# Kernel optimization log

Measured on AMD Instinct MI355X. Metric: run time of the kernel, lower is better.

Reference implementation:

```python
import jax, jax.numpy as jnp
import numpy as np

N_NODES = 100000
N_EDGES = 1600000
EMB_DIM = 128
BN_EPS = 1e-5


def setup_inputs() -> dict:
    key = jax.random.key(0)
    k = jax.random.split(key, 5)
    x = jax.random.normal(k[0], (N_NODES, EMB_DIM), dtype=jnp.float32)
    src = jax.random.randint(k[1], (N_EDGES,), 0, N_NODES)
    dst = jax.random.randint(k[2], (N_EDGES,), 0, N_NODES)
    W = jax.random.normal(k[3], (EMB_DIM, EMB_DIM), dtype=jnp.float32) / np.float32(np.sqrt(EMB_DIM))
    b = jnp.zeros((EMB_DIM,), dtype=jnp.float32)
    gamma = jnp.ones((EMB_DIM,), dtype=jnp.float32)
    beta = jnp.zeros((EMB_DIM,), dtype=jnp.float32)
    return {"x": x, "src": src, "dst": dst, "W": W, "b": b, "gamma": gamma, "beta": beta}


def reference(x, src, dst, W, b, gamma, beta):
    n = x.shape[0]
    ones = jnp.ones(src.shape, dtype=x.dtype)
    # DGL GraphConv norm='both': degrees clamped to min 1
    deg_out = jnp.maximum(jax.ops.segment_sum(ones, src, num_segments=n), 1.0)
    deg_in = jnp.maximum(jax.ops.segment_sum(ones, dst, num_segments=n), 1.0)
    norm_src = jax.lax.rsqrt(deg_out)  # [N]
    norm_dst = jax.lax.rsqrt(deg_in)   # [N]
    # W applied before aggregation (in_feats == out_feats path in DGL)
    h = (x * norm_src[:, None]) @ W                              # [N, D]
    agg = jax.ops.segment_sum(h[src], dst, num_segments=n)       # SpMM gather/scatter, [N, D]
    h = agg * norm_dst[:, None] + b                              # [N, D]
    # BatchNorm1d over nodes (training-mode batch stats, biased variance)
    mean = jnp.mean(h, axis=0)
    var = jnp.var(h, axis=0)
    h = (h - mean) * jax.lax.rsqrt(var + BN_EPS) * gamma + beta
    h = jax.nn.relu(h)
    # dropout: identity in eval-mode reference
    return h + x  # residual
```

## Files before the change

kernel.cpp:

```cpp
#include <hip/hip_runtime.h>
#include <hip/hip_bf16.h>

#define NN 100000
#define NE 1600000
#define D  128
#define BN_EPS 1e-5f

#define CB  782
#define NC  256
#define EPC (NE / NC)
#define NSLICE  4
#define SLICESZ 30800
#define SW      (SLICESZ / 2)
#define SCH     128
#define EPH (NE / SCH)

typedef __attribute__((ext_vector_type(8))) short bf16x8;
typedef __attribute__((ext_vector_type(4))) float f32x4;

#define WLD 136

static __device__ __forceinline__ ushort f2bf(float f) {
    __hip_bfloat16 b = __float2bfloat16(f);
    return *reinterpret_cast<ushort*>(&b);
}
static __device__ __forceinline__ float bflo(unsigned v) {
    return __uint_as_float((v & 0xffffu) << 16);
}
static __device__ __forceinline__ float bfhi(unsigned v) {
    return __uint_as_float(v & 0xffff0000u);
}

__global__ void k_wcast(const float* __restrict__ W, ushort* __restrict__ WT) {
    int i = blockIdx.x * 256 + threadIdx.x;
    int n = i >> 7, k = i & 127;
    WT[i] = f2bf(W[k * D + n]);
}


__global__ __launch_bounds__(256) void k_ccount(const int* __restrict__ dst,
                                                int* __restrict__ P ) {
    __shared__ int hist[CB];
    const int c = blockIdx.x;
    const int t = threadIdx.x;
    for (int i = t; i < CB; i += 256) hist[i] = 0;
    __syncthreads();
    const int base = c * EPC;
    for (int i = t; i < EPC; i += 256)
        atomicAdd(&hist[dst[base + i] >> 7], 1);
    __syncthreads();
    for (int i = t; i < CB; i += 256) P[i * NC + c] = hist[i];
}

__global__ __launch_bounds__(256) void k_cscanA(int* __restrict__ P,
                                                int* __restrict__ bintotal) {
    __shared__ int sh[NC];
    const int b = blockIdx.x;
    const int t = threadIdx.x;
    const int v = P[b * NC + t];
    sh[t] = v;
    __syncthreads();
    for (int off = 1; off < NC; off <<= 1) {
        int u = (t >= off) ? sh[t - off] : 0;
        __syncthreads();
        sh[t] += u;
        __syncthreads();
    }
    P[b * NC + t] = sh[t] - v;
    if (t == NC - 1) bintotal[b] = sh[t];
}

__global__ __launch_bounds__(1024) void k_cscanB(const int* __restrict__ bintotal,
                                                 int* __restrict__ binbase) {
    __shared__ int sh[1024];
    const int t = threadIdx.x;
    const int v = (t < CB) ? bintotal[t] : 0;
    sh[t] = v;
    __syncthreads();
    for (int off = 1; off < 1024; off <<= 1) {
        int u = (t >= off) ? sh[t - off] : 0;
        __syncthreads();
        sh[t] += u;
        __syncthreads();
    }
    if (t < CB) binbase[t] = sh[t] - v;
    if (t == CB - 1) binbase[CB] = sh[t];
}

__global__ __launch_bounds__(256) void k_cscatter(const int* __restrict__ dst,
                                                  const int* __restrict__ src,
                                                  const int* __restrict__ P,
                                                  const int* __restrict__ binbase,
                                                  int* __restrict__ sedge) {
    __shared__ int cur[CB];
    const int c = blockIdx.x;
    const int t = threadIdx.x;
    for (int i = t; i < CB; i += 256) cur[i] = binbase[i] + P[i * NC + c];
    __syncthreads();
    const int base = c * EPC;
    for (int i = t; i < EPC; i += 256) {
        int d = dst[base + i];
        int pos = atomicAdd(&cur[d >> 7], 1);
        sedge[pos] = src[base + i] | ((d & 127) << 17);
    }
}

__global__ __launch_bounds__(256) void k_fine(const int* __restrict__ sedge,
                                              const int* __restrict__ binbase,
                                              int* __restrict__ ptr,
                                              int* __restrict__ esrc) {
    __shared__ int fh[128], fp[128], fcur[128];
    const int b = blockIdx.x;
    const int t = threadIdx.x;
    const int lo = binbase[b], hi = binbase[b + 1];
    if (t < 128) fh[t] = 0;
    __syncthreads();
    for (int i = lo + t; i < hi; i += 256)
        atomicAdd(&fh[(unsigned)sedge[i] >> 17], 1);
    __syncthreads();
    if (t < 128) fp[t] = fh[t];
    __syncthreads();
    for (int off = 1; off < 128; off <<= 1) {
        int u = (t < 128 && t >= off) ? fp[t - off] : 0;
        __syncthreads();
        if (t < 128) fp[t] += u;
        __syncthreads();
    }
    if (t < 128) {
        const int node = b * 128 + t;
        const int ex = fp[t] - fh[t];
        fcur[t] = ex;
        if (node < NN) {
            ptr[node] = lo + ex;
        } else if (node == NN) {
            ptr[NN] = lo + ex;
        }
    }
    __syncthreads();
    for (int i = lo + t; i < hi; i += 256) {
        unsigned v = (unsigned)sedge[i];
        int pos = atomicAdd(&fcur[v >> 17], 1);
        esrc[lo + pos] = v & 0x1FFFF;
    }
}


__global__ __launch_bounds__(256) void k_shist(const int* __restrict__ src,
                                               int* __restrict__ SP ) {
    __shared__ int hist[SW];
    const int s = blockIdx.x / SCH;
    const int c = blockIdx.x % SCH;
    const int t = threadIdx.x;
    const int lo = s * SLICESZ;
    for (int i = t; i < SW; i += 256) hist[i] = 0;
    __syncthreads();
    const int base = c * EPH;
    for (int i = t; i < EPH; i += 256) {
        int k = src[base + i] - lo;
        if ((unsigned)k < (unsigned)SLICESZ)
            atomicAdd(&hist[k >> 1], 1 << ((k & 1) * 16));
    }
    __syncthreads();
    int* out = SP + ((size_t)s * SCH + c) * SW;
    for (int i = t; i < SW; i += 256) out[i] = hist[i];
}

__global__ void k_smerge(const int* __restrict__ SP, float* __restrict__ degout) {
    int w = blockIdx.x * 256 + threadIdx.x;
    if (w >= (NN + 1) / 2) return;
    const int n = w * 2;
    const int s = n / SLICESZ;
    const int k = n - s * SLICESZ;
    const int* col = SP + ((size_t)s * SCH) * SW + (k >> 1);
    int lo = 0, hi = 0;
#pragma unroll 8
    for (int c = 0; c < SCH; ++c) {
        int v = col[(size_t)c * SW];
        lo += v & 0xFFFF;
        hi += (v >> 16) & 0xFFFF;
    }
    degout[n] = (float)lo;
    if (n + 1 < NN) degout[n + 1] = (float)hi;
}

__global__ __launch_bounds__(256) void k_gemm(const float* __restrict__ x,
                                              const float* __restrict__ degout,
                                              const ushort* __restrict__ WT,
                                              ushort* __restrict__ h) {
    __shared__ ushort Wl[D * WLD];

    const int t = threadIdx.x;
    for (int s = t; s < 2048; s += 256) {
        int row = s >> 4, slot = s & 15;
        uint4 v = *reinterpret_cast<const uint4*>(WT + row * D + slot * 8);
        *reinterpret_cast<uint4*>(&Wl[row * WLD + slot * 8]) = v;
    }
    __syncthreads();

    const int wave = t >> 6;
    const int lane = t & 63;
    const int m16  = lane & 15;
    const int kq   = lane >> 4;
    const int row  = blockIdx.x * 64 + wave * 16 + m16;
    const int rc   = row < NN ? row : NN - 1;

    const float nrm = rsqrtf(fmaxf(degout[rc], 1.0f));

    bf16x8 afrag[4];
    const float* xr = x + (size_t)rc * D + kq * 8;
#pragma unroll
    for (int kt = 0; kt < 4; ++kt) {
        f32x4 lo = *reinterpret_cast<const f32x4*>(xr + kt * 32);
        f32x4 hi = *reinterpret_cast<const f32x4*>(xr + kt * 32 + 4);
        union { bf16x8 v; ushort u[8]; } af;
#pragma unroll
        for (int j = 0; j < 4; ++j) {
            af.u[j]     = f2bf(lo[j] * nrm);
            af.u[4 + j] = f2bf(hi[j] * nrm);
        }
        afrag[kt] = af.v;
    }

    f32x4 acc[8];
#pragma unroll
    for (int nt = 0; nt < 8; ++nt) acc[nt] = (f32x4)(0.0f);

#pragma unroll
    for (int kt = 0; kt < 4; ++kt) {
#pragma unroll
        for (int nt = 0; nt < 8; ++nt) {
            int n = nt * 16 + m16;
            const bf16x8 bfrag = *reinterpret_cast<const bf16x8*>(
                &Wl[n * WLD + kt * 32 + kq * 8]);
            acc[nt] = __builtin_amdgcn_mfma_f32_16x16x32_bf16(afrag[kt], bfrag, acc[nt], 0, 0, 0);
        }
    }

    const int orow = blockIdx.x * 64 + wave * 16 + kq * 4;
#pragma unroll
    for (int nt = 0; nt < 8; ++nt) {
#pragma unroll
        for (int r = 0; r < 4; ++r) {
            int rr = orow + r;
            if (rr < NN) h[(size_t)rr * D + nt * 16 + m16] = f2bf(acc[nt][r]);
        }
    }
}

__global__ __launch_bounds__(256) void k_agg(const ushort* __restrict__ h,
                                             const int* __restrict__ ptr,
                                             const int* __restrict__ esrc,
                                             const float* __restrict__ b,
                                             ushort* __restrict__ h2) {
    const int node = blockIdx.x * 4 + (threadIdx.x >> 6);
    const int lane = threadIdx.x & 63;
    if (node >= NN) return;
    const int s0 = ptr[node];
    const int s1 = ptr[node + 1];
    const int eg = lane >> 4;
    const int cb = (lane & 15) * 8;

    float acc[8];
#pragma unroll
    for (int j = 0; j < 8; ++j) acc[j] = 0.0f;

    for (int i = s0; i < s1; i += 16) {
        int  idx[4];
        bool p[4];
        uint4 v[4];
#pragma unroll
        for (int u = 0; u < 4; ++u) {
            int ii = i + eg + 4 * u;
            p[u] = ii < s1;
            if (p[u]) idx[u] = esrc[ii];
        }
#pragma unroll
        for (int u = 0; u < 4; ++u)
            if (p[u]) v[u] = *reinterpret_cast<const uint4*>(h + (size_t)idx[u] * D + cb);
#pragma unroll
        for (int u = 0; u < 4; ++u) {
            if (p[u]) {
                acc[0] += bflo(v[u].x); acc[1] += bfhi(v[u].x);
                acc[2] += bflo(v[u].y); acc[3] += bfhi(v[u].y);
                acc[4] += bflo(v[u].z); acc[5] += bfhi(v[u].z);
                acc[6] += bflo(v[u].w); acc[7] += bfhi(v[u].w);
            }
        }
    }
#pragma unroll
    for (int j = 0; j < 8; ++j) {
        acc[j] += __shfl_xor(acc[j], 16, 64);
        acc[j] += __shfl_xor(acc[j], 32, 64);
    }
    if (eg == 0) {
        const float nrm = rsqrtf(fmaxf((float)(s1 - s0), 1.0f));
        uint4 o;
        unsigned w[4];
#pragma unroll
        for (int m = 0; m < 4; ++m) {
            float e0 = acc[2 * m]     * nrm + b[cb + 2 * m];
            float e1 = acc[2 * m + 1] * nrm + b[cb + 2 * m + 1];
            w[m] = (unsigned)f2bf(e0) | ((unsigned)f2bf(e1) << 16);
        }
        o.x = w[0]; o.y = w[1]; o.z = w[2]; o.w = w[3];
        *reinterpret_cast<uint4*>(h2 + (size_t)node * D + cb) = o;
    }
}

__global__ __launch_bounds__(256) void k_stats(const unsigned* __restrict__ h2u,
                                               float* __restrict__ stats) {
    __shared__ float red[4][256];
    const int t = threadIdx.x;
    float s1lo = 0.f, s1hi = 0.f, s2lo = 0.f, s2hi = 0.f;
    const int total = NN * (D / 2);
    const int stride = gridDim.x * 256;
    for (int i = blockIdx.x * 256 + t; i < total; i += stride) {
        unsigned v = h2u[i];
        float lo = bflo(v), hi = bfhi(v);
        s1lo += lo; s1hi += hi;
        s2lo += lo * lo; s2hi += hi * hi;
    }
    red[0][t] = s1lo; red[1][t] = s1hi; red[2][t] = s2lo; red[3][t] = s2hi;
    __syncthreads();
    if (t < 64) {
        const int c = t * 2;
        float a0 = red[0][t] + red[0][t + 64] + red[0][t + 128] + red[0][t + 192];
        float a1 = red[1][t] + red[1][t + 64] + red[1][t + 128] + red[1][t + 192];
        float q0 = red[2][t] + red[2][t + 64] + red[2][t + 128] + red[2][t + 192];
        float q1 = red[3][t] + red[3][t + 64] + red[3][t + 128] + red[3][t + 192];
        atomicAdd(&stats[c], a0);
        atomicAdd(&stats[c + 1], a1);
        atomicAdd(&stats[128 + c], q0);
        atomicAdd(&stats[128 + c + 1], q1);
    }
}

__global__ void k_final(const uint2* __restrict__ h2v, const float4* __restrict__ xv,
                        const float* __restrict__ gamma, const float* __restrict__ beta,
                        const float* __restrict__ stats, float4* __restrict__ outv) {
    const int i = blockIdx.x * 256 + threadIdx.x;
    const int total = NN * (D / 4);
    if (i >= total) return;
    const int c = (i & 31) * 4;
    const float inv_n = 1.0f / (float)NN;
    uint2 v = h2v[i];
    float4 xx = xv[i];
    float hv[4] = { bflo(v.x), bfhi(v.x), bflo(v.y), bfhi(v.y) };
    float xr[4] = { xx.x, xx.y, xx.z, xx.w };
    float o[4];
#pragma unroll
    for (int m = 0; m < 4; ++m) {
        float mean = stats[c + m] * inv_n;
        float var  = stats[128 + c + m] * inv_n - mean * mean;
        float t = (hv[m] - mean) * rsqrtf(var + BN_EPS) * gamma[c + m] + beta[c + m];
        o[m] = fmaxf(t, 0.0f) + xr[m];
    }
    float4 ov; ov.x = o[0]; ov.y = o[1]; ov.z = o[2]; ov.w = o[3];
    outv[i] = ov;
}

extern "C" void kernel_launch(void* const* d_in, const int* in_sizes, int n_in,
                              void* d_out, int out_size, void* d_ws, size_t ws_size,
                              hipStream_t stream) {
    const float* x     = (const float*)d_in[0];
    const int*   src   = (const int*)d_in[1];
    const int*   dst   = (const int*)d_in[2];
    const float* W     = (const float*)d_in[3];
    const float* b     = (const float*)d_in[4];
    const float* gamma = (const float*)d_in[5];
    const float* beta  = (const float*)d_in[6];
    float* out = (float*)d_out;

    float* ws     = (float*)d_ws;
    ushort* h2    = (ushort*)ws;
    float* degout = ws + (size_t)NN * D;
    float* stats  = degout + NN;
    int*   ptr    = (int*)(stats + 256);
    int*   esrc   = ptr + (NN + 1);
    ushort* WT    = (ushort*)(esrc + NE);

    int* sedge    = (int*)ws;
    int* SP       = sedge + NE;
    int* P        = SP + (size_t)NSLICE * SCH * SW;
    int* bintotal = P + (size_t)CB * NC;
    int* binbase  = bintotal + CB;

    ushort* h = (ushort*)d_out;

    hipMemsetAsync(stats, 0, 256 * sizeof(float), stream);

    k_wcast<<<64, 256, 0, stream>>>(W, WT);
    k_ccount<<<NC, 256, 0, stream>>>(dst, P);
    k_cscanA<<<CB, 256, 0, stream>>>(P, bintotal);
    k_cscanB<<<1, 1024, 0, stream>>>(bintotal, binbase);
    k_cscatter<<<NC, 256, 0, stream>>>(dst, src, P, binbase, sedge);
    k_shist<<<NSLICE * SCH, 256, 0, stream>>>(src, SP);
    k_smerge<<<((NN + 1) / 2 + 255) / 256, 256, 0, stream>>>(SP, degout);
    k_gemm<<<(NN + 63) / 64, 256, 0, stream>>>(x, degout, WT, h);
    k_fine<<<CB, 256, 0, stream>>>(sedge, binbase, ptr, esrc);
    k_agg<<<(NN + 3) / 4, 256, 0, stream>>>(h, ptr, esrc, b, h2);
    k_stats<<<1024, 256, 0, stream>>>((const unsigned*)h2, stats);
    k_final<<<(NN * (D / 4) + 255) / 256, 256, 0, stream>>>((const uint2*)h2, (const float4*)x,
                                                            gamma, beta, stats, (float4*)out);
}
```

Before: 244.6 us.

## Fuse weight cast, dst bin count, src degree histogram and stats clear into one kernel

```diff
diff --git a/kernel.cpp b/kernel.cpp
--- a/kernel.cpp
+++ b/kernel.cpp
@@ -12,7 +12,7 @@
 #define NSLICE  4
 #define SLICESZ 30800
 #define SW      (SLICESZ / 2)
-#define SCH     128
+#define SCH     64
 #define EPH (NE / SCH)
 
 typedef __attribute__((ext_vector_type(8))) short bf16x8;
@@ -31,26 +31,46 @@
     return __uint_as_float(v & 0xffff0000u);
 }
 
-__global__ void k_wcast(const float* __restrict__ W, ushort* __restrict__ WT) {
-    int i = blockIdx.x * 256 + threadIdx.x;
-    int n = i >> 7, k = i & 127;
-    WT[i] = f2bf(W[k * D + n]);
-}
-
-
-__global__ __launch_bounds__(256) void k_ccount(const int* __restrict__ dst,
-                                                int* __restrict__ P ) {
-    __shared__ int hist[CB];
-    const int c = blockIdx.x;
-    const int t = threadIdx.x;
-    for (int i = t; i < CB; i += 256) hist[i] = 0;
-    __syncthreads();
-    const int base = c * EPC;
+__global__ __launch_bounds__(256) void k_front(const int* __restrict__ src,
+                                               const int* __restrict__ dst,
+                                               const float* __restrict__ W,
+                                               ushort* __restrict__ WT,
+                                               int* __restrict__ SP,
+                                               int* __restrict__ P,
+                                               float* __restrict__ stats) {
+    __shared__ int hist[SW];
+    __shared__ int dh[CB];
+    const int t = threadIdx.x;
+    const int s = blockIdx.x >> 6;
+    const int c = blockIdx.x & 63;
+    for (int i = t; i < SW; i += 256) hist[i] = 0;
+    for (int i = t; i < CB; i += 256) dh[i] = 0;
+    __syncthreads();
+
+    const int lo = s * SLICESZ;
+    const int sbase = c * EPH;
+    for (int i = t; i < EPH; i += 256) {
+        int k = src[sbase + i] - lo;
+        if ((unsigned)k < (unsigned)SLICESZ)
+            atomicAdd(&hist[k >> 1], 1 << ((k & 1) * 16));
+    }
+    const int dbase = blockIdx.x * EPC;
     for (int i = t; i < EPC; i += 256)
-        atomicAdd(&hist[dst[base + i] >> 7], 1);
-    __syncthreads();
-    for (int i = t; i < CB; i += 256) P[i * NC + c] = hist[i];
-}
+        atomicAdd(&dh[dst[dbase + i] >> 7], 1);
+    __syncthreads();
+
+    int* outS = SP + ((size_t)s * SCH + c) * SW;
+    for (int i = t; i < SW; i += 256) outS[i] = hist[i];
+    for (int i = t; i < CB; i += 256) P[i * NC + blockIdx.x] = dh[i];
+
+    if (blockIdx.x < 64) {
+        int i = blockIdx.x * 256 + t;
+        int n = i >> 7, k2 = i & 127;
+        WT[i] = f2bf(W[k2 * D + n]);
+    }
+    if (blockIdx.x == 64) stats[t] = 0.0f;
+}
+
 
 __global__ __launch_bounds__(256) void k_cscanA(int* __restrict__ P,
                                                 int* __restrict__ bintotal) {
@@ -144,26 +164,6 @@
     }
 }
 
-
-__global__ __launch_bounds__(256) void k_shist(const int* __restrict__ src,
-                                               int* __restrict__ SP ) {
-    __shared__ int hist[SW];
-    const int s = blockIdx.x / SCH;
-    const int c = blockIdx.x % SCH;
-    const int t = threadIdx.x;
-    const int lo = s * SLICESZ;
-    for (int i = t; i < SW; i += 256) hist[i] = 0;
-    __syncthreads();
-    const int base = c * EPH;
-    for (int i = t; i < EPH; i += 256) {
-        int k = src[base + i] - lo;
-        if ((unsigned)k < (unsigned)SLICESZ)
-            atomicAdd(&hist[k >> 1], 1 << ((k & 1) * 16));
-    }
-    __syncthreads();
-    int* out = SP + ((size_t)s * SCH + c) * SW;
-    for (int i = t; i < SW; i += 256) out[i] = hist[i];
-}
 
 __global__ void k_smerge(const int* __restrict__ SP, float* __restrict__ degout) {
     int w = blockIdx.x * 256 + threadIdx.x;
@@ -387,14 +387,10 @@
 
     ushort* h = (ushort*)d_out;
 
-    hipMemsetAsync(stats, 0, 256 * sizeof(float), stream);
-
-    k_wcast<<<64, 256, 0, stream>>>(W, WT);
-    k_ccount<<<NC, 256, 0, stream>>>(dst, P);
+    k_front<<<NSLICE * SCH, 256, 0, stream>>>(src, dst, W, WT, SP, P, stats);
     k_cscanA<<<CB, 256, 0, stream>>>(P, bintotal);
     k_cscanB<<<1, 1024, 0, stream>>>(bintotal, binbase);
     k_cscatter<<<NC, 256, 0, stream>>>(dst, src, P, binbase, sedge);
-    k_shist<<<NSLICE * SCH, 256, 0, stream>>>(src, SP);
     k_smerge<<<((NN + 1) / 2 + 255) / 256, 256, 0, stream>>>(SP, degout);
     k_gemm<<<(NN + 63) / 64, 256, 0, stream>>>(x, degout, WT, h);
     k_fine<<<CB, 256, 0, stream>>>(sedge, binbase, ptr, esrc);
```

Result: no change. 244.7 us (+0.0%).
